# Kernel tuning notes

Measured on AMD Instinct MI355X. Metric: run time of the kernel, lower is better.

## Reference

```python
import jax, jax.numpy as jnp
import numpy as np

N = 50000   # nodes
E = 800000  # edges (before self-loops)
IN = 128; H = 4; C = 32; HC = H * C; OUT = 47
EPS = 1e-16  # PyG softmax denominator eps
NEG_SLOPE = 0.2


def setup_inputs() -> dict:
    key = jax.random.key(0)
    ks = jax.random.split(key, 20)
    g = lambda k, shape, s=0.1: (jax.random.normal(k, shape, dtype=jnp.float32) * s)
    inp = {}
    inp["x"] = jax.random.normal(ks[0], (N, IN), dtype=jnp.float32)
    inp["edge_index"] = jax.random.randint(ks[1], (2, E), 0, N, dtype=jnp.int32)
    # layer 0: GATConv(IN -> H*C, concat=True) + skip Linear(IN -> HC)
    inp["lin_w0"] = g(ks[2], (IN, HC)); inp["att_src0"] = g(ks[3], (H, C)); inp["att_dst0"] = g(ks[4], (H, C))
    inp["bias0"] = g(ks[5], (HC,)); inp["skip_w0"] = g(ks[6], (IN, HC)); inp["skip_b0"] = g(ks[7], (HC,))
    # layer 1: GATConv(HC -> H*C, concat=True) + skip Linear(HC -> HC)
    inp["lin_w1"] = g(ks[8], (HC, HC)); inp["att_src1"] = g(ks[9], (H, C)); inp["att_dst1"] = g(ks[10], (H, C))
    inp["bias1"] = g(ks[11], (HC,)); inp["skip_w1"] = g(ks[12], (HC, HC)); inp["skip_b1"] = g(ks[13], (HC,))
    # layer 2: GATConv(HC -> OUT, heads=H, concat=False) + skip Linear(HC -> OUT)
    inp["lin_w2"] = g(ks[14], (HC, H * OUT)); inp["att_src2"] = g(ks[15], (H, OUT)); inp["att_dst2"] = g(ks[16], (H, OUT))
    inp["bias2"] = g(ks[17], (OUT,)); inp["skip_w2"] = g(ks[18], (HC, OUT)); inp["skip_b2"] = g(ks[19], (OUT,))
    return inp


def _gat_conv(x, src, dst, lin_w, att_src, att_dst, bias, concat):
    """PyG GATConv (self-loops already appended to src/dst)."""
    h, c = att_src.shape
    n = x.shape[0]
    xh = (x @ lin_w).reshape(n, h, c)                      # [N, H, C]
    a_src = jnp.einsum('nhc,hc->nh', xh, att_src)          # [N, H]
    a_dst = jnp.einsum('nhc,hc->nh', xh, att_dst)          # [N, H]
    e = a_src[src] + a_dst[dst]                            # [E', H]
    e = jax.nn.leaky_relu(e, NEG_SLOPE)
    # segment softmax over incoming edges per destination node
    m = jax.ops.segment_max(e, dst, num_segments=n)        # [N, H]
    ex = jnp.exp(e - m[dst])
    s = jax.ops.segment_sum(ex, dst, num_segments=n)       # [N, H]
    alpha = ex / (s[dst] + EPS)                            # [E', H]
    out = jax.ops.segment_sum(xh[src] * alpha[:, :, None], dst, num_segments=n)  # [N, H, C]
    out = out.reshape(n, h * c) if concat else out.mean(axis=1)
    return out + bias


def reference(x, edge_index, lin_w0, att_src0, att_dst0, bias0, skip_w0, skip_b0,
              lin_w1, att_src1, att_dst1, bias1, skip_w1, skip_b1,
              lin_w2, att_src2, att_dst2, bias2, skip_w2, skip_b2):
    n = x.shape[0]
    loop = jnp.arange(n, dtype=edge_index.dtype)
    src = jnp.concatenate([edge_index[0], loop])
    dst = jnp.concatenate([edge_index[1], loop])
    # layer 0 (+ skip, ELU; dropout is identity at inference)
    x = _gat_conv(x, src, dst, lin_w0, att_src0, att_dst0, bias0, True) + x @ skip_w0 + skip_b0
    x = jax.nn.elu(x)
    # layer 1
    x = _gat_conv(x, src, dst, lin_w1, att_src1, att_dst1, bias1, True) + x @ skip_w1 + skip_b1
    x = jax.nn.elu(x)
    # layer 2 (concat=False -> head mean), no activation
    x = _gat_conv(x, src, dst, lin_w2, att_src2, att_dst2, bias2, False) + x @ skip_w2 + skip_b2
    return x
```

## Files before the change

kernel.cpp:

```cpp
#include <hip/hip_runtime.h>
#include <math.h>
#include <type_traits>

#define KD 128
#define HC 128
#define NF2 188
#define NF2PB 192
#define OUTC 47

typedef __attribute__((ext_vector_type(8))) __bf16 bf16x8;
typedef __attribute__((ext_vector_type(4))) float f32x4;
typedef __attribute__((ext_vector_type(2))) float f32x2;

#ifdef __has_builtin
#if __has_builtin(__builtin_amdgcn_cvt_pk_f32_fp8)
#define HAVE_CVT_FP8_DEC 1
#endif
#if __has_builtin(__builtin_amdgcn_cvt_pk_fp8_f32)
#define HAVE_CVT_FP8_ENC 1
#endif
#endif

__device__ inline float bfhi_to_f(unsigned int u) {
    union { unsigned int u; float f; } c; c.u = u & 0xFFFF0000u; return c.f;
}
__device__ inline float bflo_to_f(unsigned int u) {
    union { unsigned int u; float f; } c; c.u = u << 16; return c.f;
}
__device__ inline unsigned short f_to_bfu(float f) {
    return __builtin_bit_cast(unsigned short, (__bf16)f);
}
__device__ inline unsigned int pk_bf(float a, float b) {
    return (unsigned int)f_to_bfu(a) | ((unsigned int)f_to_bfu(b) << 16);
}

__device__ inline void dot2bf(float& acc, unsigned int x, unsigned int a) {
    asm("v_dot2_f32_bf16 %0, %1, %2, %0" : "+v"(acc) : "v"(x), "v"(a));
}
__device__ inline unsigned int permb(unsigned int hi, unsigned int lo, unsigned int sel) {
    return __builtin_amdgcn_perm(hi, lo, sel);
}

#ifndef HAVE_CVT_FP8_DEC
__device__ inline float fp8_to_f32_b(unsigned int b) {
    int e = (b >> 3) & 15, m = b & 7;
    float v = e ? ldexpf((float)(8 + m), e - 10) : ldexpf((float)m, -9);
    return (b & 0x80) ? -v : v;
}
#endif
__device__ inline void fp8x4_dec(unsigned int q, float& a, float& b, float& c, float& d) {
#ifdef HAVE_CVT_FP8_DEC
    f32x2 lo = __builtin_amdgcn_cvt_pk_f32_fp8((int)q, false);
    f32x2 hi = __builtin_amdgcn_cvt_pk_f32_fp8((int)q, true);
    a = lo[0]; b = lo[1]; c = hi[0]; d = hi[1];
#else
    a = fp8_to_f32_b(q & 0xFF); b = fp8_to_f32_b((q >> 8) & 0xFF);
    c = fp8_to_f32_b((q >> 16) & 0xFF); d = fp8_to_f32_b((q >> 24) & 0xFF);
#endif
}
__device__ inline unsigned char f32_to_fp8(float v) {
#ifdef HAVE_CVT_FP8_ENC
    return (unsigned char)(__builtin_amdgcn_cvt_pk_fp8_f32(v, v, 0, false) & 0xFF);
#else
    unsigned u = __builtin_bit_cast(unsigned, v);
    unsigned s = (u >> 24) & 0x80;
    float a = fabsf(v);
    if (a < 0.0009765625f) return (unsigned char)s;
    if (a >= 448.f) return (unsigned char)(s | 0x7E);
    int e; float m = frexpf(a, &e);
    int E = e - 1 + 7;
    int mi = (int)rintf(m * 16.f);
    if (mi == 16) { mi = 8; ++E; if (E >= 16) return (unsigned char)(s | 0x7E); }
    if (E <= 0) {
        int q = (int)rintf(a * 512.f); if (q > 7) q = 7;
        return (unsigned char)(s | q);
    }
    return (unsigned char)(s | (E << 3) | (mi - 8));
#endif
}
__device__ inline float fp8dot(unsigned int q, float4 al, float acc) {
    float a, b, c, d;
    fp8x4_dec(q, a, b, c, d);
    return acc + al.x * a + al.y * b + al.z * c + al.w * d;
}

#define NPART 8
#define EPB 2048

__global__ __launch_bounds__(256) void count_kernel(
    const int* __restrict__ dst, int* deg, int e, int rngsz) {
    int r = blockIdx.x & (NPART - 1);
    int chunk = blockIdx.x / NPART;
    int base = chunk * EPB + threadIdx.x * 8;
    int lo = r * rngsz, hi = lo + rngsz;
    if (base >= e) return;
    if (base + 7 < e) {
        int4 d0 = *(const int4*)(dst + base);
        int4 d1 = *(const int4*)(dst + base + 4);
        int dd[8] = {d0.x, d0.y, d0.z, d0.w, d1.x, d1.y, d1.z, d1.w};
#pragma unroll
        for (int k = 0; k < 8; ++k)
            if (dd[k] >= lo && dd[k] < hi) atomicAdd(&deg[dd[k]], 1);
    } else {
        for (int k = base; k < e; ++k) {
            int d = dst[k];
            if (d >= lo && d < hi) atomicAdd(&deg[d], 1);
        }
    }
}

__global__ __launch_bounds__(256) void scan_base_kernel(
    int* __restrict__ deg, int* counter,
    int* __restrict__ row_ptr, int* __restrict__ fill, int* __restrict__ col, int n) {
    int i = blockIdx.x * 256 + threadIdx.x;
    int v = (i < n) ? (deg[i] + 1) : 0;
    int lane = threadIdx.x & 63, w = threadIdx.x >> 6;
    int incl = v;
#pragma unroll
    for (int off = 1; off < 64; off <<= 1) {
        int u = __shfl_up(incl, off, 64);
        if (lane >= off) incl += u;
    }
    __shared__ int wsum[4];
    __shared__ int base_sh;
    if (lane == 63) wsum[w] = incl;
    __syncthreads();
    if (threadIdx.x == 0)
        base_sh = atomicAdd(counter, wsum[0] + wsum[1] + wsum[2] + wsum[3]);
    int woff = 0;
    for (int k = 0; k < w; ++k) woff += wsum[k];
    __syncthreads();
    int excl = base_sh + woff + incl - v;
    if (i < n) {
        row_ptr[i] = excl;
        col[excl] = i;
        fill[i] = excl + 1;
        deg[i] = v;
    }
}

__global__ __launch_bounds__(256) void fill_kernel(
    const int* __restrict__ ei, int* fill, int* col, int e, int rngsz) {
    int r = blockIdx.x & (NPART - 1);
    int chunk = blockIdx.x / NPART;
    int base = chunk * EPB + threadIdx.x * 8;
    int lo = r * rngsz, hi = lo + rngsz;
    if (base >= e) return;
    const int* dstp = ei + e;
    if (base + 7 < e) {
        int4 d0 = *(const int4*)(dstp + base);
        int4 d1 = *(const int4*)(dstp + base + 4);
        int dd[8] = {d0.x, d0.y, d0.z, d0.w, d1.x, d1.y, d1.z, d1.w};
#pragma unroll
        for (int k = 0; k < 8; ++k) {
            if (dd[k] >= lo && dd[k] < hi) {
                int pos = atomicAdd(&fill[dd[k]], 1);
                col[pos] = ei[base + k];
            }
        }
    } else {
        for (int k = base; k < e; ++k) {
            int d = dstp[k];
            if (d >= lo && d < hi) {
                int pos = atomicAdd(&fill[d], 1);
                col[pos] = ei[k];
            }
        }
    }
}

__global__ __launch_bounds__(256) void prep_w_kernel(
    const float* __restrict__ lw0, const float* __restrict__ sw0,
    const float* __restrict__ lw1, const float* __restrict__ sw1,
    const float* __restrict__ lw2, const float* __restrict__ sw2,
    __bf16* __restrict__ bt) {
    int idx = blockIdx.x * 256 + threadIdx.x;
    int buf = idx >> 15;
    int r = idx & 32767;
    int n = r >> 7, k = r & 127;
    float v = 0.f;
    if (buf == 0) v = (n < 128) ? lw0[k * 128 + n] : sw0[k * 128 + n - 128];
    else if (buf == 1) v = (n < 128) ? lw1[k * 128 + n] : sw1[k * 128 + n - 128];
    else {
        if (n < 188) v = lw2[k * 188 + n];
        else if (n >= 192 && n < 239) v = sw2[k * 47 + n - 192];
    }
    bt[idx] = (__bf16)v;
}

template <typename AT, typename SKT, int NLIN, int NSK, int TR>
__global__ __launch_bounds__(256) void gemm_fused_kernel(
    const AT* __restrict__ A, const __bf16* __restrict__ Bt,
    void* __restrict__ out0, int N0, int ldc0,
    const float* __restrict__ bias1, SKT* __restrict__ out1, int N1, int M) {
    __shared__ __bf16 As[64][136];
    __shared__ __bf16 Bs[64][136];
    int tid = threadIdx.x;
    int m0 = blockIdx.x * 64;

#pragma unroll
    for (int rep = 0; rep < 4; ++rep) {
        int idx = tid + rep * 256;
        int row = idx >> 4, seg = idx & 15;
        int gm = m0 + row;
        bf16x8 v = {};
        if (gm < M) {
            if constexpr (std::is_same<AT, float>::value) {
                const float* p = A + gm * KD + seg * 8;
                float4 f0 = *(const float4*)p;
                float4 f1 = *(const float4*)(p + 4);
                v[0] = (__bf16)f0.x; v[1] = (__bf16)f0.y; v[2] = (__bf16)f0.z; v[3] = (__bf16)f0.w;
                v[4] = (__bf16)f1.x; v[5] = (__bf16)f1.y; v[6] = (__bf16)f1.z; v[7] = (__bf16)f1.w;
            } else {
                v = *(const bf16x8*)(A + gm * KD + seg * 8);
            }
        }
        *(bf16x8*)&As[row][seg * 8] = v;
    }
    __syncthreads();

    int w = tid >> 6, lane = tid & 63;
    int lr = lane & 15, quad = lane >> 4;

#pragma unroll
    for (int t = 0; t < NLIN + NSK; ++t) {
        bool second = t >= NLIN;
        int N = second ? N1 : N0;
        int n0 = (second ? (t - NLIN) : t) * 64;
        if (t) __syncthreads();
#pragma unroll
        for (int rep = 0; rep < 4; ++rep) {
            int idx = tid + rep * 256;
            int row = idx >> 4, seg = idx & 15;
            *(bf16x8*)&Bs[row][seg * 8] =
                *(const bf16x8*)(Bt + ((t * 64 + row) << 7) + seg * 8);
        }
        __syncthreads();

        f32x4 acc[4] = {};
#pragma unroll
        for (int kc = 0; kc < 128; kc += 32) {
            bf16x8 a0 = *(const bf16x8*)&As[w * 16 + lr][kc + quad * 8];
            bf16x8 b0 = *(const bf16x8*)&Bs[lr][kc + quad * 8];
            bf16x8 b1 = *(const bf16x8*)&Bs[16 + lr][kc + quad * 8];
            bf16x8 b2 = *(const bf16x8*)&Bs[32 + lr][kc + quad * 8];
            bf16x8 b3 = *(const bf16x8*)&Bs[48 + lr][kc + quad * 8];
            acc[0] = __builtin_amdgcn_mfma_f32_16x16x32_bf16(a0, b0, acc[0], 0, 0, 0);
            acc[1] = __builtin_amdgcn_mfma_f32_16x16x32_bf16(a0, b1, acc[1], 0, 0, 0);
            acc[2] = __builtin_amdgcn_mfma_f32_16x16x32_bf16(a0, b2, acc[2], 0, 0, 0);
            acc[3] = __builtin_amdgcn_mfma_f32_16x16x32_bf16(a0, b3, acc[3], 0, 0, 0);
        }
#pragma unroll
        for (int c = 0; c < 4; ++c) {
#pragma unroll
            for (int reg = 0; reg < 4; ++reg) {
                int row = m0 + w * 16 + quad * 4 + reg;
                int colg = n0 + c * 16 + lr;
                if (row < M && colg < N) {
                    float v = acc[c][reg];
                    if (second) {
                        v += bias1[colg];
                        out1[row * N + colg] = (SKT)v;
                    } else if (TR) {
                        int h = (colg * 1395) >> 16;
                        ((unsigned char*)out0)[row * ldc0 + (colg - 47 * h) * 4 + h] =
                            f32_to_fp8(v);
                    } else {
                        ((__bf16*)out0)[row * ldc0 + colg] = (__bf16)v;
                    }
                }
            }
        }
    }
}

__global__ __launch_bounds__(256) void att_kernel(
    const __bf16* __restrict__ xh, const float* __restrict__ att_s,
    const float* __restrict__ att_d, float* __restrict__ a_src,
    float* __restrict__ a_dst, int n) {
    int tid = blockIdx.x * 256 + threadIdx.x;
    int node = tid >> 4;
    int l16 = threadIdx.x & 15;
    if (node >= n) return;
    uint4 q = ((const uint4*)xh)[node * 16 + l16];
    int f0 = l16 * 8;
    float4 as0 = *(const float4*)(att_s + f0);
    float4 as1 = *(const float4*)(att_s + f0 + 4);
    float4 ad0 = *(const float4*)(att_d + f0);
    float4 ad1 = *(const float4*)(att_d + f0 + 4);
    float x0 = bflo_to_f(q.x), x1 = bfhi_to_f(q.x);
    float x2 = bflo_to_f(q.y), x3 = bfhi_to_f(q.y);
    float x4 = bflo_to_f(q.z), x5 = bfhi_to_f(q.z);
    float x6 = bflo_to_f(q.w), x7 = bfhi_to_f(q.w);
    float hs = x0 * as0.x + x1 * as0.y + x2 * as0.z + x3 * as0.w
             + x4 * as1.x + x5 * as1.y + x6 * as1.z + x7 * as1.w;
    float hd = x0 * ad0.x + x1 * ad0.y + x2 * ad0.z + x3 * ad0.w
             + x4 * ad1.x + x5 * ad1.y + x6 * ad1.z + x7 * ad1.w;
    hs += __shfl_xor(hs, 1, 64); hs += __shfl_xor(hs, 2, 64);
    hd += __shfl_xor(hd, 1, 64); hd += __shfl_xor(hd, 2, 64);
    if ((l16 & 3) == 0) {
        int h = l16 >> 2;
        a_src[node * 4 + h] = hs;
        a_dst[node * 4 + h] = hd;
    }
}

__global__ __launch_bounds__(256) void att2_kernel(
    const unsigned char* __restrict__ xh8, const float* __restrict__ att_s,
    const float* __restrict__ att_d, float* __restrict__ a_src,
    float* __restrict__ a_dst, int n) {
    int node = (blockIdx.x * 256 + threadIdx.x) >> 6;
    int lane = threadIdx.x & 63;
    if (node >= n) return;
    float ps0 = 0.f, ps1 = 0.f, ps2 = 0.f, ps3 = 0.f;
    float pd0 = 0.f, pd1 = 0.f, pd2 = 0.f, pd3 = 0.f;
    if (lane < 47) {
        unsigned int q = ((const unsigned int*)(xh8 + node * NF2PB))[lane];
        float x0, x1, x2, x3;
        fp8x4_dec(q, x0, x1, x2, x3);
        ps0 = x0 * att_s[lane];       ps1 = x1 * att_s[47 + lane];
        ps2 = x2 * att_s[94 + lane];  ps3 = x3 * att_s[141 + lane];
        pd0 = x0 * att_d[lane];       pd1 = x1 * att_d[47 + lane];
        pd2 = x2 * att_d[94 + lane];  pd3 = x3 * att_d[141 + lane];
    }
#pragma unroll
    for (int off = 1; off <= 32; off <<= 1) {
        ps0 += __shfl_xor(ps0, off, 64); ps1 += __shfl_xor(ps1, off, 64);
        ps2 += __shfl_xor(ps2, off, 64); ps3 += __shfl_xor(ps3, off, 64);
        pd0 += __shfl_xor(pd0, off, 64); pd1 += __shfl_xor(pd1, off, 64);
        pd2 += __shfl_xor(pd2, off, 64); pd3 += __shfl_xor(pd3, off, 64);
    }
    if (lane < 4) {
        float vs = (lane == 0) ? ps0 : (lane == 1) ? ps1 : (lane == 2) ? ps2 : ps3;
        float vd = (lane == 0) ? pd0 : (lane == 1) ? pd1 : (lane == 2) ? pd2 : pd3;
        a_src[node * 4 + lane] = vs;
        a_dst[node * 4 + lane] = vd;
    }
}

__global__ __launch_bounds__(256) void agg0_kernel(
    const uint4* __restrict__ xh, const float* __restrict__ a_src,
    const float* __restrict__ a_dst, const uint4* __restrict__ skipb,
    const float* __restrict__ bias, const int* __restrict__ row_ptr,
    const int* __restrict__ deg, const int* __restrict__ col,
    uint4* __restrict__ outp, int n) {
    __shared__ int s_j[16][16];
    __shared__ unsigned s_ap[16][8][4];
    int grp = threadIdx.x >> 4;
    int l16 = threadIdx.x & 15;
    int node = (blockIdx.x << 4) + grp;
    bool active = node < n;
    int node_c = active ? node : 0;
    int start = row_ptr[node_c];
    int end = start + (active ? deg[node_c] : 0);
    float4 ad4 = *(const float4*)(a_dst + 4 * node_c);

    float s0 = 0.f, s1 = 0.f, s2 = 0.f, s3 = 0.f;
    float e00 = 0.f, e01 = 0.f, e02 = 0.f, e03 = 0.f;
    float e10 = 0.f, e11 = 0.f, e12 = 0.f, e13 = 0.f;
    int jc0 = 0, jc1 = 0;
    int c = 0;
    for (int base = start; base < end; base += 16, ++c) {
        int e = base + l16;
        bool ok = e < end;
        int j = ok ? col[e] : 0;
        float4 as4 = *(const float4*)(a_src + 4 * j);
        float v0 = as4.x + ad4.x; v0 = v0 > 0.f ? v0 : 0.2f * v0;
        float v1 = as4.y + ad4.y; v1 = v1 > 0.f ? v1 : 0.2f * v1;
        float v2 = as4.z + ad4.z; v2 = v2 > 0.f ? v2 : 0.2f * v2;
        float v3 = as4.w + ad4.w; v3 = v3 > 0.f ? v3 : 0.2f * v3;
        float x0 = ok ? __expf(v0) : 0.f;
        float x1 = ok ? __expf(v1) : 0.f;
        float x2 = ok ? __expf(v2) : 0.f;
        float x3 = ok ? __expf(v3) : 0.f;
        s0 += x0; s1 += x1; s2 += x2; s3 += x3;
        if (c == 0) { jc0 = j; e00 = x0; e01 = x1; e02 = x2; e03 = x3; }
        else if (c == 1) { jc1 = j; e10 = x0; e11 = x1; e12 = x2; e13 = x3; }
    }
#pragma unroll
    for (int off = 1; off <= 8; off <<= 1) {
        s0 += __shfl_xor(s0, off, 64);
        s1 += __shfl_xor(s1, off, 64);
        s2 += __shfl_xor(s2, off, 64);
        s3 += __shfl_xor(s3, off, 64);
    }
    float i0 = 1.f / (s0 + 1e-16f), i1 = 1.f / (s1 + 1e-16f);
    float i2 = 1.f / (s2 + 1e-16f), i3 = 1.f / (s3 + 1e-16f);

    int myh = l16 >> 2;
    float a0 = 0.f, a1 = 0.f, a2 = 0.f, a3 = 0.f;
    float a4 = 0.f, a5 = 0.f, a6 = 0.f, a7 = 0.f;
    c = 0;
    for (int base = start; base < end; base += 16, ++c) {
        float al0, al1, al2, al3; int jv;
        if (c == 0) {
            jv = jc0; al0 = e00 * i0; al1 = e01 * i1; al2 = e02 * i2; al3 = e03 * i3;
        } else if (c == 1) {
            jv = jc1; al0 = e10 * i0; al1 = e11 * i1; al2 = e12 * i2; al3 = e13 * i3;
        } else {
            int e = base + l16;
            bool ok = e < end;
            jv = ok ? col[e] : 0;
            float4 as4 = *(const float4*)(a_src + 4 * jv);
            float v0 = as4.x + ad4.x; v0 = v0 > 0.f ? v0 : 0.2f * v0;
            float v1 = as4.y + ad4.y; v1 = v1 > 0.f ? v1 : 0.2f * v1;
            float v2 = as4.z + ad4.z; v2 = v2 > 0.f ? v2 : 0.2f * v2;
            float v3 = as4.w + ad4.w; v3 = v3 > 0.f ? v3 : 0.2f * v3;
            al0 = ok ? __expf(v0) * i0 : 0.f;
            al1 = ok ? __expf(v1) * i1 : 0.f;
            al2 = ok ? __expf(v2) * i2 : 0.f;
            al3 = ok ? __expf(v3) * i3 : 0.f;
        }
        s_j[grp][l16] = jv;
        float o0 = __shfl_xor(al0, 1, 64);
        float o1 = __shfl_xor(al1, 1, 64);
        float o2 = __shfl_xor(al2, 1, 64);
        float o3 = __shfl_xor(al3, 1, 64);
        if (!(l16 & 1)) {
            *(uint4*)&s_ap[grp][l16 >> 1][0] =
                make_uint4(pk_bf(al0, o0), pk_bf(al1, o1), pk_bf(al2, o2), pk_bf(al3, o3));
        }
        int cnt = end - base; if (cnt > 16) cnt = 16;
        int npair = (cnt + 1) >> 1;
        int p = 0;
        for (; p + 1 < npair; p += 2) {
            int2 jpa = *(const int2*)&s_j[grp][2 * p];
            int2 jpb = *(const int2*)&s_j[grp][2 * p + 2];
            unsigned apa = s_ap[grp][p][myh];
            unsigned apb = s_ap[grp][p + 1][myh];
            uint4 qa0 = xh[jpa.x * 16 + l16];
            uint4 qb0 = xh[jpa.y * 16 + l16];
            uint4 qa1 = xh[jpb.x * 16 + l16];
            uint4 qb1 = xh[jpb.y * 16 + l16];
            dot2bf(a0, permb(qb0.x, qa0.x, 0x05040100u), apa);
            dot2bf(a1, permb(qb0.x, qa0.x, 0x07060302u), apa);
            dot2bf(a2, permb(qb0.y, qa0.y, 0x05040100u), apa);
            dot2bf(a3, permb(qb0.y, qa0.y, 0x07060302u), apa);
            dot2bf(a4, permb(qb0.z, qa0.z, 0x05040100u), apa);
            dot2bf(a5, permb(qb0.z, qa0.z, 0x07060302u), apa);
            dot2bf(a6, permb(qb0.w, qa0.w, 0x05040100u), apa);
            dot2bf(a7, permb(qb0.w, qa0.w, 0x07060302u), apa);
            dot2bf(a0, permb(qb1.x, qa1.x, 0x05040100u), apb);
            dot2bf(a1, permb(qb1.x, qa1.x, 0x07060302u), apb);
            dot2bf(a2, permb(qb1.y, qa1.y, 0x05040100u), apb);
            dot2bf(a3, permb(qb1.y, qa1.y, 0x07060302u), apb);
            dot2bf(a4, permb(qb1.z, qa1.z, 0x05040100u), apb);
            dot2bf(a5, permb(qb1.z, qa1.z, 0x07060302u), apb);
            dot2bf(a6, permb(qb1.w, qa1.w, 0x05040100u), apb);
            dot2bf(a7, permb(qb1.w, qa1.w, 0x07060302u), apb);
        }
        for (; p < npair; ++p) {
            int2 jp = *(const int2*)&s_j[grp][2 * p];
            unsigned ap = s_ap[grp][p][myh];
            uint4 qa = xh[jp.x * 16 + l16];
            uint4 qb = xh[jp.y * 16 + l16];
            dot2bf(a0, permb(qb.x, qa.x, 0x05040100u), ap);
            dot2bf(a1, permb(qb.x, qa.x, 0x07060302u), ap);
            dot2bf(a2, permb(qb.y, qa.y, 0x05040100u), ap);
            dot2bf(a3, permb(qb.y, qa.y, 0x07060302u), ap);
            dot2bf(a4, permb(qb.z, qa.z, 0x05040100u), ap);
            dot2bf(a5, permb(qb.z, qa.z, 0x07060302u), ap);
            dot2bf(a6, permb(qb.w, qa.w, 0x05040100u), ap);
            dot2bf(a7, permb(qb.w, qa.w, 0x07060302u), ap);
        }
    }

    if (active) {
        float4 b0 = *(const float4*)(bias + 8 * l16);
        float4 b1 = *(const float4*)(bias + 8 * l16 + 4);
        uint4 skq = skipb[node * 16 + l16];
        float v0 = a0 + b0.x + bflo_to_f(skq.x);
        float v1 = a1 + b0.y + bfhi_to_f(skq.x);
        float v2 = a2 + b0.z + bflo_to_f(skq.y);
        float v3 = a3 + b0.w + bfhi_to_f(skq.y);
        float v4 = a4 + b1.x + bflo_to_f(skq.z);
        float v5 = a5 + b1.y + bfhi_to_f(skq.z);
        float v6 = a6 + b1.z + bflo_to_f(skq.w);
        float v7 = a7 + b1.w + bfhi_to_f(skq.w);
        v0 = v0 > 0.f ? v0 : (__expf(v0) - 1.f);
        v1 = v1 > 0.f ? v1 : (__expf(v1) - 1.f);
        v2 = v2 > 0.f ? v2 : (__expf(v2) - 1.f);
        v3 = v3 > 0.f ? v3 : (__expf(v3) - 1.f);
        v4 = v4 > 0.f ? v4 : (__expf(v4) - 1.f);
        v5 = v5 > 0.f ? v5 : (__expf(v5) - 1.f);
        v6 = v6 > 0.f ? v6 : (__expf(v6) - 1.f);
        v7 = v7 > 0.f ? v7 : (__expf(v7) - 1.f);
        outp[node * 16 + l16] =
            make_uint4(pk_bf(v0, v1), pk_bf(v2, v3), pk_bf(v4, v5), pk_bf(v6, v7));
    }
}

__global__ __launch_bounds__(256) void agg1_kernel(
    const unsigned int* __restrict__ x8, const float* __restrict__ a_src,
    const float* __restrict__ a_dst, const float* __restrict__ skip,
    const float* __restrict__ bias, const int* __restrict__ row_ptr,
    const int* __restrict__ deg, const int* __restrict__ col,
    float* __restrict__ outp, int n) {
    __shared__ float s_af[4][64][4];
    __shared__ int s_j[4][64];
    int w = threadIdx.x >> 6;
    int lane = threadIdx.x & 63;
    int node = (blockIdx.x << 2) + w;
    bool active = node < n;
    int node_c = active ? node : 0;
    int start = row_ptr[node_c];
    int end = start + (active ? deg[node_c] : 0);
    float4 ad4 = *(const float4*)(a_dst + 4 * node_c);
    float adh[4] = {ad4.x, ad4.y, ad4.z, ad4.w};

    int e0 = start + lane;
    bool ok0 = e0 < end;
    int jcap = ok0 ? col[e0] : 0;
    float evc[4];
    {
        float4 as4 = *(const float4*)(a_src + 4 * jcap);
        float v0 = as4.x + adh[0]; v0 = v0 > 0.f ? v0 : 0.2f * v0;
        float v1 = as4.y + adh[1]; v1 = v1 > 0.f ? v1 : 0.2f * v1;
        float v2 = as4.z + adh[2]; v2 = v2 > 0.f ? v2 : 0.2f * v2;
        float v3 = as4.w + adh[3]; v3 = v3 > 0.f ? v3 : 0.2f * v3;
        evc[0] = ok0 ? __expf(v0) : 0.f;
        evc[1] = ok0 ? __expf(v1) : 0.f;
        evc[2] = ok0 ? __expf(v2) : 0.f;
        evc[3] = ok0 ? __expf(v3) : 0.f;
    }
    float s[4] = {evc[0], evc[1], evc[2], evc[3]};
    for (int e = e0 + 64; e < end; e += 64) {
        int j = col[e];
        float4 as4 = *(const float4*)(a_src + 4 * j);
        float ev[4] = {as4.x + adh[0], as4.y + adh[1], as4.z + adh[2], as4.w + adh[3]};
#pragma unroll
        for (int h = 0; h < 4; ++h) {
            float v = ev[h] > 0.f ? ev[h] : 0.2f * ev[h];
            s[h] += __expf(v);
        }
    }
#pragma unroll
    for (int off = 32; off >= 1; off >>= 1)
#pragma unroll
        for (int h = 0; h < 4; ++h) s[h] += __shfl_xor(s[h], off, 64);
    float inv[4];
#pragma unroll
    for (int h = 0; h < 4; ++h) inv[h] = 1.f / (s[h] + 1e-16f);

    bool lv = lane < 47;
    float acc0 = 0.f;

    auto run_chunk = [&](int cnt) {
        int t = 0;
        for (; t + 7 < cnt; t += 8) {
            unsigned int q0 = lv ? x8[s_j[w][t] * 48 + lane] : 0u;
            unsigned int q1 = lv ? x8[s_j[w][t + 1] * 48 + lane] : 0u;
            unsigned int q2 = lv ? x8[s_j[w][t + 2] * 48 + lane] : 0u;
            unsigned int q3 = lv ? x8[s_j[w][t + 3] * 48 + lane] : 0u;
            unsigned int q4 = lv ? x8[s_j[w][t + 4] * 48 + lane] : 0u;
            unsigned int q5 = lv ? x8[s_j[w][t + 5] * 48 + lane] : 0u;
            unsigned int q6 = lv ? x8[s_j[w][t + 6] * 48 + lane] : 0u;
            unsigned int q7 = lv ? x8[s_j[w][t + 7] * 48 + lane] : 0u;
            acc0 = fp8dot(q0, *(const float4*)&s_af[w][t][0], acc0);
            acc0 = fp8dot(q1, *(const float4*)&s_af[w][t + 1][0], acc0);
            acc0 = fp8dot(q2, *(const float4*)&s_af[w][t + 2][0], acc0);
            acc0 = fp8dot(q3, *(const float4*)&s_af[w][t + 3][0], acc0);
            acc0 = fp8dot(q4, *(const float4*)&s_af[w][t + 4][0], acc0);
            acc0 = fp8dot(q5, *(const float4*)&s_af[w][t + 5][0], acc0);
            acc0 = fp8dot(q6, *(const float4*)&s_af[w][t + 6][0], acc0);
            acc0 = fp8dot(q7, *(const float4*)&s_af[w][t + 7][0], acc0);
        }
        for (; t + 3 < cnt; t += 4) {
            unsigned int q0 = lv ? x8[s_j[w][t] * 48 + lane] : 0u;
            unsigned int q1 = lv ? x8[s_j[w][t + 1] * 48 + lane] : 0u;
            unsigned int q2 = lv ? x8[s_j[w][t + 2] * 48 + lane] : 0u;
            unsigned int q3 = lv ? x8[s_j[w][t + 3] * 48 + lane] : 0u;
            acc0 = fp8dot(q0, *(const float4*)&s_af[w][t][0], acc0);
            acc0 = fp8dot(q1, *(const float4*)&s_af[w][t + 1][0], acc0);
            acc0 = fp8dot(q2, *(const float4*)&s_af[w][t + 2][0], acc0);
            acc0 = fp8dot(q3, *(const float4*)&s_af[w][t + 3][0], acc0);
        }
        for (; t < cnt; ++t) {
            unsigned int q = lv ? x8[s_j[w][t] * 48 + lane] : 0u;
            acc0 = fp8dot(q, *(const float4*)&s_af[w][t][0], acc0);
        }
    };

    {
        float al[4];
#pragma unroll
        for (int h = 0; h < 4; ++h) al[h] = evc[h] * inv[h];
        s_j[w][lane] = jcap;
        *(float4*)&s_af[w][lane][0] = make_float4(al[0], al[1], al[2], al[3]);
        int cnt = end - start; if (cnt > 64) cnt = 64;
        run_chunk(cnt);
    }
    for (int base = start + 64; base < end; base += 64) {
        int e = base + lane;
        bool ok = e < end;
        int jv = ok ? col[e] : 0;
        float4 as4 = *(const float4*)(a_src + 4 * jv);
        float al[4];
#pragma unroll
        for (int h = 0; h < 4; ++h) {
            float ev = ((const float*)&as4)[h] + adh[h];
            ev = ev > 0.f ? ev : 0.2f * ev;
            al[h] = ok ? __expf(ev) * inv[h] : 0.f;
        }
        s_j[w][lane] = jv;
        *(float4*)&s_af[w][lane][0] = make_float4(al[0], al[1], al[2], al[3]);
        int cnt = end - base; if (cnt > 64) cnt = 64;
        run_chunk(cnt);
    }

    if (active && lane < OUTC) {
        float v = acc0 * 0.25f + bias[lane] + skip[node * OUTC + lane];
        outp[node * OUTC + lane] = v;
    }
}

extern "C" void kernel_launch(void* const* d_in, const int* in_sizes, int n_in,
                              void* d_out, int out_size, void* d_ws, size_t ws_size,
                              hipStream_t stream) {
    const float* x        = (const float*)d_in[0];
    const int*   ei       = (const int*)d_in[1];
    const float* lin_w0   = (const float*)d_in[2];
    const float* att_src0 = (const float*)d_in[3];
    const float* att_dst0 = (const float*)d_in[4];
    const float* bias0    = (const float*)d_in[5];
    const float* skip_w0  = (const float*)d_in[6];
    const float* skip_b0  = (const float*)d_in[7];
    const float* lin_w1   = (const float*)d_in[8];
    const float* att_src1 = (const float*)d_in[9];
    const float* att_dst1 = (const float*)d_in[10];
    const float* bias1    = (const float*)d_in[11];
    const float* skip_w1  = (const float*)d_in[12];
    const float* skip_b1  = (const float*)d_in[13];
    const float* lin_w2   = (const float*)d_in[14];
    const float* att_src2 = (const float*)d_in[15];
    const float* att_dst2 = (const float*)d_in[16];
    const float* bias2    = (const float*)d_in[17];
    const float* skip_w2  = (const float*)d_in[18];
    const float* skip_b2  = (const float*)d_in[19];
    float* out = (float*)d_out;

    const int N = in_sizes[0] / KD;
    const int E = in_sizes[1] / 2;
    const int ET_ = E + N;

    char* ws = (char*)d_ws;
    size_t off = 0;
    auto alloc = [&](size_t bytes) -> void* {
        void* p = ws + off;
        off = (off + bytes + 255) & ~(size_t)255;
        return p;
    };
    void*   xh      = alloc((size_t)N * HC * 2 + 256);
    __bf16* buf_bf  = (__bf16*)alloc((size_t)N * HC * 2);
    void*   skipbuf = alloc((size_t)N * HC * 4);
    float* a_src    = (float*)alloc((size_t)N * 4 * 4);
    float* a_dst    = (float*)alloc((size_t)N * 4 * 4);
    int* deg        = (int*)alloc((size_t)N * 4);
    int* row_ptr    = (int*)alloc((size_t)N * 4);
    int* fill       = (int*)alloc((size_t)N * 4);
    int* col        = (int*)alloc((size_t)ET_ * 4);
    int* counter    = (int*)alloc(256);
    __bf16* Bt      = (__bf16*)alloc((size_t)3 * 256 * 128 * 2);

    prep_w_kernel<<<384, 256, 0, stream>>>(lin_w0, skip_w0, lin_w1, skip_w1,
                                           lin_w2, skip_w2, Bt);

    hipMemsetAsync(deg, 0, (size_t)N * 4, stream);
    hipMemsetAsync(counter, 0, 4, stream);
    int rngsz = (N + NPART - 1) / NPART;
    int cblocks = ((E + EPB - 1) / EPB) * NPART;
    count_kernel<<<cblocks, 256, 0, stream>>>(ei + E, deg, E, rngsz);
    scan_base_kernel<<<(N + 255) / 256, 256, 0, stream>>>(deg, counter, row_ptr, fill, col, N);
    fill_kernel<<<cblocks, 256, 0, stream>>>(ei, fill, col, E, rngsz);

    dim3 blk(256);
    int mblocks = (N + 63) / 64;
    int wave_blocks = (N + 3) / 4;
    int grp_blocks = (N + 15) / 16;
    int att_blocks = (N * 16 + 255) / 256;

    gemm_fused_kernel<float, __bf16, 2, 2, 0><<<mblocks, blk, 0, stream>>>(
        x, Bt, xh, HC, HC, skip_b0, (__bf16*)skipbuf, HC, N);
    att_kernel<<<att_blocks, blk, 0, stream>>>((const __bf16*)xh, att_src0, att_dst0,
                                               a_src, a_dst, N);
    agg0_kernel<<<grp_blocks, blk, 0, stream>>>((const uint4*)xh, a_src, a_dst,
                                                (const uint4*)skipbuf, bias0,
                                                row_ptr, deg, col, (uint4*)buf_bf, N);
    gemm_fused_kernel<__bf16, __bf16, 2, 2, 0><<<mblocks, blk, 0, stream>>>(
        buf_bf, Bt + 32768, xh, HC, HC, skip_b1, (__bf16*)skipbuf, HC, N);
    att_kernel<<<att_blocks, blk, 0, stream>>>((const __bf16*)xh, att_src1, att_dst1,
                                               a_src, a_dst, N);
    agg0_kernel<<<grp_blocks, blk, 0, stream>>>((const uint4*)xh, a_src, a_dst,
                                                (const uint4*)skipbuf, bias1,
                                                row_ptr, deg, col, (uint4*)buf_bf, N);
    gemm_fused_kernel<__bf16, float, 3, 1, 1><<<mblocks, blk, 0, stream>>>(
        buf_bf, Bt + 65536, xh, NF2, NF2PB, skip_b2, (float*)skipbuf, OUTC, N);
    att2_kernel<<<wave_blocks, blk, 0, stream>>>((const unsigned char*)xh, att_src2,
                                                 att_dst2, a_src, a_dst, N);
    agg1_kernel<<<wave_blocks, blk, 0, stream>>>((const unsigned int*)xh, a_src, a_dst,
                                                 (const float*)skipbuf, bias2,
                                                 row_ptr, deg, col, out, N);
}
```

Baseline: 386.0 us.

## Split GAT aggregation into per-edge alpha kernel and per-head-quarter gather kernel

The fused layer-0/1 aggregation kernel is replaced by two kernels. The first computes the softmax attention weights per edge and writes them to a bf16 per-head edge array. The second gathers neighbour features, with each block quarter handling one head slice and four lanes per node. The aim is to remove the LDS staging and intra-group serialization of the fused kernel and to expose more independent gathers. In exchange it adds an extra launch, a write and re-read of the alpha array, and requires padding on the col array. It also halves the skip buffer allocation.

```diff
diff --git a/kernel.cpp b/kernel.cpp
--- a/kernel.cpp
+++ b/kernel.cpp
@@ -338,14 +338,11 @@
     }
 }
 
-__global__ __launch_bounds__(256) void agg0_kernel(
-    const uint4* __restrict__ xh, const float* __restrict__ a_src,
-    const float* __restrict__ a_dst, const uint4* __restrict__ skipb,
-    const float* __restrict__ bias, const int* __restrict__ row_ptr,
-    const int* __restrict__ deg, const int* __restrict__ col,
-    uint4* __restrict__ outp, int n) {
-    __shared__ int s_j[16][16];
-    __shared__ unsigned s_ap[16][8][4];
+__global__ __launch_bounds__(256) void alpha2_kernel(
+    const float* __restrict__ a_src, const float* __restrict__ a_dst,
+    const int* __restrict__ row_ptr, const int* __restrict__ deg,
+    const int* __restrict__ col, unsigned short* __restrict__ alp,
+    int epad, int n) {
     int grp = threadIdx.x >> 4;
     int l16 = threadIdx.x & 15;
     int node = (blockIdx.x << 4) + grp;
@@ -358,7 +355,6 @@
     float s0 = 0.f, s1 = 0.f, s2 = 0.f, s3 = 0.f;
     float e00 = 0.f, e01 = 0.f, e02 = 0.f, e03 = 0.f;
     float e10 = 0.f, e11 = 0.f, e12 = 0.f, e13 = 0.f;
-    int jc0 = 0, jc1 = 0;
     int c = 0;
     for (int base = start; base < end; base += 16, ++c) {
         int e = base + l16;
@@ -374,8 +370,8 @@
         float x2 = ok ? __expf(v2) : 0.f;
         float x3 = ok ? __expf(v3) : 0.f;
         s0 += x0; s1 += x1; s2 += x2; s3 += x3;
-        if (c == 0) { jc0 = j; e00 = x0; e01 = x1; e02 = x2; e03 = x3; }
-        else if (c == 1) { jc1 = j; e10 = x0; e11 = x1; e12 = x2; e13 = x3; }
+        if (c == 0) { e00 = x0; e01 = x1; e02 = x2; e03 = x3; }
+        else if (c == 1) { e10 = x0; e11 = x1; e12 = x2; e13 = x3; }
     }
 #pragma unroll
     for (int off = 1; off <= 8; off <<= 1) {
@@ -387,21 +383,18 @@
     float i0 = 1.f / (s0 + 1e-16f), i1 = 1.f / (s1 + 1e-16f);
     float i2 = 1.f / (s2 + 1e-16f), i3 = 1.f / (s3 + 1e-16f);
 
-    int myh = l16 >> 2;
-    float a0 = 0.f, a1 = 0.f, a2 = 0.f, a3 = 0.f;
-    float a4 = 0.f, a5 = 0.f, a6 = 0.f, a7 = 0.f;
     c = 0;
     for (int base = start; base < end; base += 16, ++c) {
-        float al0, al1, al2, al3; int jv;
+        float al0, al1, al2, al3;
         if (c == 0) {
-            jv = jc0; al0 = e00 * i0; al1 = e01 * i1; al2 = e02 * i2; al3 = e03 * i3;
+            al0 = e00 * i0; al1 = e01 * i1; al2 = e02 * i2; al3 = e03 * i3;
         } else if (c == 1) {
-            jv = jc1; al0 = e10 * i0; al1 = e11 * i1; al2 = e12 * i2; al3 = e13 * i3;
+            al0 = e10 * i0; al1 = e11 * i1; al2 = e12 * i2; al3 = e13 * i3;
         } else {
             int e = base + l16;
             bool ok = e < end;
-            jv = ok ? col[e] : 0;
-            float4 as4 = *(const float4*)(a_src + 4 * jv);
+            int j = ok ? col[e] : 0;
+            float4 as4 = *(const float4*)(a_src + 4 * j);
             float v0 = as4.x + ad4.x; v0 = v0 > 0.f ? v0 : 0.2f * v0;
             float v1 = as4.y + ad4.y; v1 = v1 > 0.f ? v1 : 0.2f * v1;
             float v2 = as4.z + ad4.z; v2 = v2 > 0.f ? v2 : 0.2f * v2;
@@ -411,83 +404,76 @@
             al2 = ok ? __expf(v2) * i2 : 0.f;
             al3 = ok ? __expf(v3) * i3 : 0.f;
         }
-        s_j[grp][l16] = jv;
-        float o0 = __shfl_xor(al0, 1, 64);
-        float o1 = __shfl_xor(al1, 1, 64);
-        float o2 = __shfl_xor(al2, 1, 64);
-        float o3 = __shfl_xor(al3, 1, 64);
-        if (!(l16 & 1)) {
-            *(uint4*)&s_ap[grp][l16 >> 1][0] =
-                make_uint4(pk_bf(al0, o0), pk_bf(al1, o1), pk_bf(al2, o2), pk_bf(al3, o3));
-        }
-        int cnt = end - base; if (cnt > 16) cnt = 16;
-        int npair = (cnt + 1) >> 1;
-        int p = 0;
-        for (; p + 1 < npair; p += 2) {
-            int2 jpa = *(const int2*)&s_j[grp][2 * p];
-            int2 jpb = *(const int2*)&s_j[grp][2 * p + 2];
-            unsigned apa = s_ap[grp][p][myh];
-            unsigned apb = s_ap[grp][p + 1][myh];
-            uint4 qa0 = xh[jpa.x * 16 + l16];
-            uint4 qb0 = xh[jpa.y * 16 + l16];
-            uint4 qa1 = xh[jpb.x * 16 + l16];
-            uint4 qb1 = xh[jpb.y * 16 + l16];
-            dot2bf(a0, permb(qb0.x, qa0.x, 0x05040100u), apa);
-            dot2bf(a1, permb(qb0.x, qa0.x, 0x07060302u), apa);
-            dot2bf(a2, permb(qb0.y, qa0.y, 0x05040100u), apa);
-            dot2bf(a3, permb(qb0.y, qa0.y, 0x07060302u), apa);
-            dot2bf(a4, permb(qb0.z, qa0.z, 0x05040100u), apa);
-            dot2bf(a5, permb(qb0.z, qa0.z, 0x07060302u), apa);
-            dot2bf(a6, permb(qb0.w, qa0.w, 0x05040100u), apa);
-            dot2bf(a7, permb(qb0.w, qa0.w, 0x07060302u), apa);
-            dot2bf(a0, permb(qb1.x, qa1.x, 0x05040100u), apb);
-            dot2bf(a1, permb(qb1.x, qa1.x, 0x07060302u), apb);
-            dot2bf(a2, permb(qb1.y, qa1.y, 0x05040100u), apb);
-            dot2bf(a3, permb(qb1.y, qa1.y, 0x07060302u), apb);
-            dot2bf(a4, permb(qb1.z, qa1.z, 0x05040100u), apb);
-            dot2bf(a5, permb(qb1.z, qa1.z, 0x07060302u), apb);
-            dot2bf(a6, permb(qb1.w, qa1.w, 0x05040100u), apb);
-            dot2bf(a7, permb(qb1.w, qa1.w, 0x07060302u), apb);
-        }
-        for (; p < npair; ++p) {
-            int2 jp = *(const int2*)&s_j[grp][2 * p];
-            unsigned ap = s_ap[grp][p][myh];
-            uint4 qa = xh[jp.x * 16 + l16];
-            uint4 qb = xh[jp.y * 16 + l16];
-            dot2bf(a0, permb(qb.x, qa.x, 0x05040100u), ap);
-            dot2bf(a1, permb(qb.x, qa.x, 0x07060302u), ap);
-            dot2bf(a2, permb(qb.y, qa.y, 0x05040100u), ap);
-            dot2bf(a3, permb(qb.y, qa.y, 0x07060302u), ap);
-            dot2bf(a4, permb(qb.z, qa.z, 0x05040100u), ap);
-            dot2bf(a5, permb(qb.z, qa.z, 0x07060302u), ap);
-            dot2bf(a6, permb(qb.w, qa.w, 0x05040100u), ap);
-            dot2bf(a7, permb(qb.w, qa.w, 0x07060302u), ap);
-        }
-    }
-
-    if (active) {
-        float4 b0 = *(const float4*)(bias + 8 * l16);
-        float4 b1 = *(const float4*)(bias + 8 * l16 + 4);
-        uint4 skq = skipb[node * 16 + l16];
-        float v0 = a0 + b0.x + bflo_to_f(skq.x);
-        float v1 = a1 + b0.y + bfhi_to_f(skq.x);
-        float v2 = a2 + b0.z + bflo_to_f(skq.y);
-        float v3 = a3 + b0.w + bfhi_to_f(skq.y);
-        float v4 = a4 + b1.x + bflo_to_f(skq.z);
-        float v5 = a5 + b1.y + bfhi_to_f(skq.z);
-        float v6 = a6 + b1.z + bflo_to_f(skq.w);
-        float v7 = a7 + b1.w + bfhi_to_f(skq.w);
-        v0 = v0 > 0.f ? v0 : (__expf(v0) - 1.f);
-        v1 = v1 > 0.f ? v1 : (__expf(v1) - 1.f);
-        v2 = v2 > 0.f ? v2 : (__expf(v2) - 1.f);
-        v3 = v3 > 0.f ? v3 : (__expf(v3) - 1.f);
-        v4 = v4 > 0.f ? v4 : (__expf(v4) - 1.f);
-        v5 = v5 > 0.f ? v5 : (__expf(v5) - 1.f);
-        v6 = v6 > 0.f ? v6 : (__expf(v6) - 1.f);
-        v7 = v7 > 0.f ? v7 : (__expf(v7) - 1.f);
-        outp[node * 16 + l16] =
-            make_uint4(pk_bf(v0, v1), pk_bf(v2, v3), pk_bf(v4, v5), pk_bf(v6, v7));
-    }
+        int e = base + l16;
+        if (active && e < end) {
+            alp[e]            = f_to_bfu(al0);
+            alp[epad + e]     = f_to_bfu(al1);
+            alp[2 * epad + e] = f_to_bfu(al2);
+            alp[3 * epad + e] = f_to_bfu(al3);
+        }
+    }
+}
+
+__global__ __launch_bounds__(256) void gather2_kernel(
+    const uint4* __restrict__ xh, const unsigned short* __restrict__ alp,
+    int epad, const uint4* __restrict__ skipb, const float* __restrict__ bias,
+    const int* __restrict__ row_ptr, const int* __restrict__ deg,
+    const int* __restrict__ col, uint4* __restrict__ outp, int n) {
+    int q = blockIdx.x & 3;
+    int nb = blockIdx.x >> 2;
+    int node = nb * 64 + (threadIdx.x >> 2);
+    if (node >= n) return;
+    int l4 = threadIdx.x & 3;
+    int s = row_ptr[node];
+    int cnt = deg[node];
+    int end = s + cnt;
+    int k0 = s >> 1, kend = (end - 1) >> 1;
+    unsigned m0 = (s & 1) ? 0xFFFF0000u : 0xFFFFFFFFu;
+    unsigned mL = (end & 1) ? 0x0000FFFFu : 0xFFFFFFFFu;
+    const unsigned* alq = (const unsigned*)(alp + (size_t)q * epad);
+    int xoff = q * 4 + l4;
+
+    float a0 = 0.f, a1 = 0.f, a2 = 0.f, a3 = 0.f;
+    float a4 = 0.f, a5 = 0.f, a6 = 0.f, a7 = 0.f;
+    for (int k = k0; k <= kend; ++k) {
+        unsigned au = alq[k];
+        if (k == k0) au &= m0;
+        if (k == kend) au &= mL;
+        int2 jj = *(const int2*)(col + 2 * k);
+        uint4 qa = xh[jj.x * 16 + xoff];
+        uint4 qb = xh[jj.y * 16 + xoff];
+        dot2bf(a0, permb(qb.x, qa.x, 0x05040100u), au);
+        dot2bf(a1, permb(qb.x, qa.x, 0x07060302u), au);
+        dot2bf(a2, permb(qb.y, qa.y, 0x05040100u), au);
+        dot2bf(a3, permb(qb.y, qa.y, 0x07060302u), au);
+        dot2bf(a4, permb(qb.z, qa.z, 0x05040100u), au);
+        dot2bf(a5, permb(qb.z, qa.z, 0x07060302u), au);
+        dot2bf(a6, permb(qb.w, qa.w, 0x05040100u), au);
+        dot2bf(a7, permb(qb.w, qa.w, 0x07060302u), au);
+    }
+
+    int f = q * 32 + l4 * 8;
+    float4 b0 = *(const float4*)(bias + f);
+    float4 b1 = *(const float4*)(bias + f + 4);
+    uint4 skq = skipb[node * 16 + xoff];
+    float v0 = a0 + b0.x + bflo_to_f(skq.x);
+    float v1 = a1 + b0.y + bfhi_to_f(skq.x);
+    float v2 = a2 + b0.z + bflo_to_f(skq.y);
+    float v3 = a3 + b0.w + bfhi_to_f(skq.y);
+    float v4 = a4 + b1.x + bflo_to_f(skq.z);
+    float v5 = a5 + b1.y + bfhi_to_f(skq.z);
+    float v6 = a6 + b1.z + bflo_to_f(skq.w);
+    float v7 = a7 + b1.w + bfhi_to_f(skq.w);
+    v0 = v0 > 0.f ? v0 : (__expf(v0) - 1.f);
+    v1 = v1 > 0.f ? v1 : (__expf(v1) - 1.f);
+    v2 = v2 > 0.f ? v2 : (__expf(v2) - 1.f);
+    v3 = v3 > 0.f ? v3 : (__expf(v3) - 1.f);
+    v4 = v4 > 0.f ? v4 : (__expf(v4) - 1.f);
+    v5 = v5 > 0.f ? v5 : (__expf(v5) - 1.f);
+    v6 = v6 > 0.f ? v6 : (__expf(v6) - 1.f);
+    v7 = v7 > 0.f ? v7 : (__expf(v7) - 1.f);
+    outp[node * 16 + xoff] =
+        make_uint4(pk_bf(v0, v1), pk_bf(v2, v3), pk_bf(v4, v5), pk_bf(v6, v7));
 }
 
 __global__ __launch_bounds__(256) void agg1_kernel(
@@ -652,21 +638,24 @@
     };
     void*   xh      = alloc((size_t)N * HC * 2 + 256);
     __bf16* buf_bf  = (__bf16*)alloc((size_t)N * HC * 2);
-    void*   skipbuf = alloc((size_t)N * HC * 4);
+    void*   skipbuf = alloc((size_t)N * HC * 2);
     float* a_src    = (float*)alloc((size_t)N * 4 * 4);
     float* a_dst    = (float*)alloc((size_t)N * 4 * 4);
     int* deg        = (int*)alloc((size_t)N * 4);
     int* row_ptr    = (int*)alloc((size_t)N * 4);
     int* fill       = (int*)alloc((size_t)N * 4);
-    int* col        = (int*)alloc((size_t)ET_ * 4);
+    int* col        = (int*)alloc((size_t)(ET_ + 16) * 4);
     int* counter    = (int*)alloc(256);
     __bf16* Bt      = (__bf16*)alloc((size_t)3 * 256 * 128 * 2);
+    int epad        = (ET_ + 64) & ~63;
+    unsigned short* alp = (unsigned short*)alloc((size_t)4 * epad * 2);
 
     prep_w_kernel<<<384, 256, 0, stream>>>(lin_w0, skip_w0, lin_w1, skip_w1,
                                            lin_w2, skip_w2, Bt);
 
     hipMemsetAsync(deg, 0, (size_t)N * 4, stream);
     hipMemsetAsync(counter, 0, 4, stream);
+    hipMemsetAsync(col + ET_, 0, 64, stream);
     int rngsz = (N + NPART - 1) / NPART;
     int cblocks = ((E + EPB - 1) / EPB) * NPART;
     count_kernel<<<cblocks, 256, 0, stream>>>(ei + E, deg, E, rngsz);
@@ -676,23 +665,30 @@
     dim3 blk(256);
     int mblocks = (N + 63) / 64;
     int wave_blocks = (N + 3) / 4;
-    int grp_blocks = (N + 15) / 16;
+    int a_blocks = (N + 15) / 16;
+    int g_blocks = ((N + 63) / 64) * 4;
     int att_blocks = (N * 16 + 255) / 256;
 
     gemm_fused_kernel<float, __bf16, 2, 2, 0><<<mblocks, blk, 0, stream>>>(
         x, Bt, xh, HC, HC, skip_b0, (__bf16*)skipbuf, HC, N);
     att_kernel<<<att_blocks, blk, 0, stream>>>((const __bf16*)xh, att_src0, att_dst0,
                                                a_src, a_dst, N);
-    agg0_kernel<<<grp_blocks, blk, 0, stream>>>((const uint4*)xh, a_src, a_dst,
-                                                (const uint4*)skipbuf, bias0,
-                                                row_ptr, deg, col, (uint4*)buf_bf, N);
+    alpha2_kernel<<<a_blocks, blk, 0, stream>>>(a_src, a_dst, row_ptr, deg, col,
+                                                alp, epad, N);
+    gather2_kernel<<<g_blocks, blk, 0, stream>>>((const uint4*)xh, alp, epad,
+                                                 (const uint4*)skipbuf, bias0,
+                                                 row_ptr, deg, col,
+                                                 (uint4*)buf_bf, N);
     gemm_fused_kernel<__bf16, __bf16, 2, 2, 0><<<mblocks, blk, 0, stream>>>(
         buf_bf, Bt + 32768, xh, HC, HC, skip_b1, (__bf16*)skipbuf, HC, N);
     att_kernel<<<att_blocks, blk, 0, stream>>>((const __bf16*)xh, att_src1, att_dst1,
                                                a_src, a_dst, N);
-    agg0_kernel<<<grp_blocks, blk, 0, stream>>>((const uint4*)xh, a_src, a_dst,
-                                                (const uint4*)skipbuf, bias1,
-                                                row_ptr, deg, col, (uint4*)buf_bf, N);
+    alpha2_kernel<<<a_blocks, blk, 0, stream>>>(a_src, a_dst, row_ptr, deg, col,
+                                                alp, epad, N);
+    gather2_kernel<<<g_blocks, blk, 0, stream>>>((const uint4*)xh, alp, epad,
+                                                 (const uint4*)skipbuf, bias1,
+                                                 row_ptr, deg, col,
+                                                 (uint4*)buf_bf, N);
     gemm_fused_kernel<__bf16, float, 3, 1, 1><<<mblocks, blk, 0, stream>>>(
         buf_bf, Bt + 65536, xh, NF2, NF2PB, skip_b2, (float*)skipbuf, OUTC, N);
     att2_kernel<<<wave_blocks, blk, 0, stream>>>((const unsigned char*)xh, att_src2,
```

Measured after the change: 460.9 us. +19.4%, slower.
